# Kernel optimization log

Measured on AMD Instinct MI355X. Metric: run time of the kernel, lower is better.

Reference implementation:

```python
import jax, jax.numpy as jnp
from jax import lax
import numpy as np

DIM = 8          # per-head dim
BN_EPS = 1e-5
ATT_EPS = 1e-15


def setup_inputs() -> dict:
    key = jax.random.key(0)
    ks = jax.random.split(key, 6)
    B, C, H, W = 2, 512, 128, 128
    total_dim = 512                      # heads(64) * dim(8)
    c3 = 3 * total_dim                   # 1536
    x = jax.random.normal(ks[0], (B, C, H, W), dtype=jnp.float32)
    w_qkv = jax.random.normal(ks[1], (c3, C), dtype=jnp.float32) * 0.02
    w_dw = jax.random.normal(ks[2], (c3, 1, 5, 5), dtype=jnp.float32) * 0.05
    w_pw = jax.random.normal(ks[3], (c3, 8, 1, 1), dtype=jnp.float32) * 0.1
    w_proj = jax.random.normal(ks[4], (512, 2 * total_dim), dtype=jnp.float32) * 0.02
    bn_gamma = jnp.ones((512,), jnp.float32)
    bn_beta = jnp.zeros((512,), jnp.float32)
    bn_mean = jnp.zeros((512,), jnp.float32)
    bn_var = jnp.ones((512,), jnp.float32)
    return {"x": x, "w_qkv": w_qkv, "w_dw": w_dw, "w_pw": w_pw, "w_proj": w_proj,
            "bn_gamma": bn_gamma, "bn_beta": bn_beta, "bn_mean": bn_mean, "bn_var": bn_var}


def reference(x, w_qkv, w_dw, w_pw, w_proj, bn_gamma, bn_beta, bn_mean, bn_var):
    B, C, H, W = x.shape
    dn = ('NCHW', 'OIHW', 'NCHW')
    # qkv: 1x1 conv, no bias/norm/act
    qkv = jnp.einsum('bchw,oc->bohw', x, w_qkv)  # (B, 1536, H, W)
    # multi-scale aggregation: 5x5 depthwise + 1x1 grouped (groups = 3*heads = 192)
    y = lax.conv_general_dilated(qkv, w_dw, (1, 1), [(2, 2), (2, 2)],
                                 feature_group_count=w_dw.shape[0], dimension_numbers=dn)
    y = lax.conv_general_dilated(y, w_pw, (1, 1), [(0, 0), (0, 0)],
                                 feature_group_count=w_pw.shape[0] // w_pw.shape[1],
                                 dimension_numbers=dn)
    mqkv = jnp.concatenate([qkv, y], axis=1)  # (B, 3072, H, W)
    N = H * W
    mqkv = mqkv.reshape(B, -1, 3 * DIM, N)    # (B, 128 heads, 24, N)
    q = jax.nn.relu(mqkv[:, :, :DIM])          # (B, h, d, N)
    k = jax.nn.relu(mqkv[:, :, DIM:2 * DIM])   # (B, h, d, N)
    v = mqkv[:, :, 2 * DIM:]                   # (B, h, d, N)
    v = jnp.pad(v, ((0, 0), (0, 0), (0, 1), (0, 0)), constant_values=1.0)  # (B,h,d+1,N)
    vk = jnp.einsum('bhdn,bhen->bhde', v, k)   # v @ k^T : (B,h,d+1,d)
    out = jnp.einsum('bhde,bhen->bhdn', vk, q)  # (B,h,d+1,N)
    out = out[:, :, :-1] / (out[:, :, -1:] + ATT_EPS)  # (B,h,d,N)
    out = out.reshape(B, -1, H, W)             # (B, 1024, H, W)
    # proj: 1x1 conv + bn2d (inference-mode affine), no act
    out = jnp.einsum('bchw,oc->bohw', out, w_proj)
    inv = bn_gamma / jnp.sqrt(bn_var + BN_EPS)
    out = out * inv[None, :, None, None] + (bn_beta - bn_mean * inv)[None, :, None, None]
    return out
```

## Files before the change

### kernel.cpp

```cpp
#include <hip/hip_runtime.h>

typedef __bf16 bf16_t;
typedef __bf16 bf16x8 __attribute__((ext_vector_type(8)));
typedef float  f32x4  __attribute__((ext_vector_type(4)));
typedef _Float16 h16;
typedef _Float16 h16x2 __attribute__((ext_vector_type(2)));
typedef _Float16 h16x4 __attribute__((ext_vector_type(4)));
typedef _Float16 h16x8 __attribute__((ext_vector_type(8)));

#define DEVINL __device__ __forceinline__

static constexpr size_t N_PIX = 16384;
static constexpr float  FIX_TAU = 2.5e-3f;

static constexpr size_t OFF_QB  = 0;
static constexpr size_t SZ_QB   = (size_t)512 * N_PIX * 2;
static constexpr size_t OFF_KV  = OFF_QB + SZ_QB;
static constexpr size_t SZ_KV   = (size_t)1024 * N_PIX * 2;
static constexpr size_t OFF_Y   = OFF_KV + SZ_KV;
static constexpr size_t SZ_Y    = (size_t)1536 * N_PIX * 2;
static constexpr size_t OFF_ATT = OFF_Y + SZ_Y;
static constexpr size_t SZ_ATT  = (size_t)N_PIX * 1024 * 2;
static constexpr size_t OFF_XT  = OFF_ATT;
static constexpr size_t OFF_XTL = OFF_ATT + (size_t)N_PIX * 512 * 2;
static constexpr size_t OFF_WALL= OFF_ATT + SZ_ATT;
static constexpr size_t SZ_WALL = (size_t)1536 * 512 * 2;
static constexpr size_t OFF_WP  = OFF_WALL + SZ_WALL;
static constexpr size_t SZ_WP   = (size_t)512 * 1024 * 2;
static constexpr size_t OFF_VK  = OFF_WP + SZ_WP;
static constexpr size_t SZ_VK   = (size_t)128 * 72 * 4;
static constexpr size_t OFF_VKP = OFF_VK + SZ_VK;
static constexpr size_t SZ_VKP  = (size_t)128 * 8 * 72 * 4;
static constexpr size_t OFF_BNA = OFF_VKP + SZ_VKP;
static constexpr size_t OFF_ZP  = OFF_BNA + 2048;
static constexpr size_t OFF_W2  = OFF_ZP + 64;
static constexpr size_t SZ_W2   = (size_t)512 * 1024 * 2;
static constexpr size_t WS_NEEDED = OFF_W2 + SZ_W2;

DEVINL void gload16(const void* g, void* l) {
  __builtin_amdgcn_global_load_lds((const __attribute__((address_space(1))) void*)g,
                                   (__attribute__((address_space(3))) void*)l, 16, 0, 0);
}

__global__ __launch_bounds__(256)
void xpose_kernel(const float* __restrict__ x, h16* __restrict__ xT, h16* __restrict__ xTl) {
  __shared__ float t[32][33];
  const int n0 = blockIdx.x * 32, c0 = blockIdx.y * 32;
  const int tx = threadIdx.x & 31, ty = threadIdx.x >> 5;
#pragma unroll
  for (int r = 0; r < 4; ++r)
    t[ty + r * 8][tx] = x[(size_t)(c0 + ty + r * 8) * N_PIX + n0 + tx];
  __syncthreads();
  const int nl = threadIdx.x >> 3, sub = threadIdx.x & 7;
  const int c8 = (sub & 3) * 8, plane = sub >> 2;
  h16x8 o;
#pragma unroll
  for (int k = 0; k < 8; ++k) {
    const float v = t[c8 + k][nl];
    if (plane == 0) {
      o[k] = (h16)v;
    } else {
      const h16 hi = (h16)v;
      o[k] = (h16)(v - (float)hi);
    }
  }
  h16* dst = plane ? xTl : xT;
  *(h16x8*)&dst[(size_t)(n0 + nl) * 512 + c0 + c8] = o;
}

static constexpr int PREP_P1 = 1536 * 512;
static constexpr int PREP_P2 = 512 * 1024;
static constexpr int PREP_TOT = PREP_P1 + PREP_P2 + 512 + 16;
__global__ __launch_bounds__(256)
void prep_kernel(const float* __restrict__ wq, const float* __restrict__ wp,
                 const float* __restrict__ gam, const float* __restrict__ bet,
                 const float* __restrict__ mu, const float* __restrict__ va,
                 h16* __restrict__ wall, bf16_t* __restrict__ wpb,
                 float* __restrict__ bna, float* __restrict__ zp) {
  const int i = blockIdx.x * 256 + threadIdx.x;
  if (i < PREP_P1) {
    const int r = i >> 9, c = i & 511;
    int o;
    if (r < 512)       o = (r >> 3) * 24 + (r & 7);
    else if (r < 1024) o = ((r - 512) >> 3) * 24 + 8 + (r & 7);
    else               o = ((r - 1024) >> 3) * 24 + 16 + (r & 7);
    wall[i] = (h16)wq[(size_t)o * 512 + c];
  } else if (i < PREP_P1 + PREP_P2) {
    const int j = i - PREP_P1;
    const int m = j >> 10;
    const float inv = gam[m] / sqrtf(va[m] + 1e-5f);
    wpb[j] = (bf16_t)(wp[j] * inv);
  } else if (i < PREP_P1 + PREP_P2 + 512) {
    const int k = i - PREP_P1 - PREP_P2;
    const float inv = gam[k] / sqrtf(va[k] + 1e-5f);
    bna[k] = bet[k] - mu[k] * inv;
  } else if (i < PREP_TOT) {
    zp[i - (PREP_P1 + PREP_P2 + 512)] = 0.f;
  }
}

__global__ __launch_bounds__(256, 2)
void gemm_qkv_kernel(const h16* __restrict__ wall, const h16* __restrict__ xT,
                     h16* __restrict__ Qb, h16* __restrict__ KV) {
  __shared__ __align__(16) h16 As[128 * 64];
  __shared__ __align__(16) h16 Bs[256 * 64];
  const int tid = threadIdx.x, wid = tid >> 6, lane = tid & 63;
  const int fr = lane & 15, fg = lane >> 4;
  const int wm = (wid >> 1) * 64, wn = (wid & 1) * 128;
  const int by = blockIdx.y;
  const bool isQ = by < 4;
  const int m0 = (isQ ? by : by - 4) * 128;
  const int n0 = blockIdx.x * 256;
  const h16* Aptr = wall + (size_t)by * 128 * 512;

  f32x4 acc[4][8] = {};

  for (int kk = 0; kk < 512; kk += 64) {
    __syncthreads();
#pragma unroll
    for (int r = 0; r < 4; ++r) {
      const int c = wid * 64 + lane + 256 * r;
      const int row = c >> 3, cc = c & 7;
      gload16(Aptr + (size_t)row * 512 + kk + ((cc ^ (row & 7)) * 8),
              As + (size_t)(wid * 64 + 256 * r) * 8);
    }
#pragma unroll
    for (int r = 0; r < 8; ++r) {
      const int c = wid * 64 + lane + 256 * r;
      const int row = c >> 3, cc = c & 7;
      gload16(xT + (size_t)(n0 + row) * 512 + kk + ((cc ^ (row & 7)) * 8),
              Bs + (size_t)(wid * 64 + 256 * r) * 8);
    }
    __syncthreads();
#pragma unroll
    for (int ks = 0; ks < 2; ++ks) {
      h16x8 af[4], bfr[8];
#pragma unroll
      for (int i = 0; i < 4; ++i)
        af[i]  = *(const h16x8*)&As[(wm + i * 16 + fr) * 64 + (((ks * 4 + fg) ^ (fr & 7)) * 8)];
#pragma unroll
      for (int j = 0; j < 8; ++j)
        bfr[j] = *(const h16x8*)&Bs[(wn + j * 16 + fr) * 64 + (((ks * 4 + fg) ^ (fr & 7)) * 8)];
#pragma unroll
      for (int i = 0; i < 4; ++i)
#pragma unroll
        for (int j = 0; j < 8; ++j)
          acc[i][j] = __builtin_amdgcn_mfma_f32_16x16x32_f16(af[i], bfr[j], acc[i][j], 0, 0, 0);
    }
  }

#pragma unroll
  for (int i = 0; i < 4; ++i)
#pragma unroll
    for (int r = 0; r < 4; ++r) {
      const int m = m0 + wm + i * 16 + fg * 4 + r;
      h16* dst = isQ ? Qb : KV;
#pragma unroll
      for (int j = 0; j < 8; ++j) {
        const int n = n0 + wn + j * 16 + fr;
        dst[(size_t)m * N_PIX + n] = (h16)acc[i][j][r];
      }
    }
}

__global__ __launch_bounds__(256)
void fix_kernel(const float* __restrict__ wq, const h16* __restrict__ xT,
                const h16* __restrict__ xTl, h16* __restrict__ Qb) {
  const int h = blockIdx.y;
  const int n = blockIdx.x * 256 + threadIdx.x;
  const int lane = threadIdx.x & 63;
  float mx = 0.f;
#pragma unroll
  for (int e = 0; e < 8; ++e)
    mx = fmaxf(mx, (float)Qb[(size_t)(h * 8 + e) * N_PIX + n]);
  unsigned long long mask = __ballot(mx < FIX_TAU);
  const int cb = blockIdx.x * 256 + ((int)threadIdx.x & ~63);
  while (mask) {
    const int bit = __builtin_ctzll(mask);
    mask &= mask - 1;
    const int np = cb + bit;
    const int c0 = lane * 8;
    const h16x8 xh = *(const h16x8*)&xT[(size_t)np * 512 + c0];
    const h16x8 xl = *(const h16x8*)&xTl[(size_t)np * 512 + c0];
    float xs[8];
#pragma unroll
    for (int u = 0; u < 8; ++u) xs[u] = (float)xh[u] + (float)xl[u];
    float acc[8];
#pragma unroll
    for (int e = 0; e < 8; ++e) {
      const float4 w0 = *(const float4*)&wq[(size_t)(h * 24 + e) * 512 + c0];
      const float4 w1 = *(const float4*)&wq[(size_t)(h * 24 + e) * 512 + c0 + 4];
      acc[e] = w0.x * xs[0] + w0.y * xs[1] + w0.z * xs[2] + w0.w * xs[3]
             + w1.x * xs[4] + w1.y * xs[5] + w1.z * xs[6] + w1.w * xs[7];
    }
#pragma unroll
    for (int e = 0; e < 8; ++e) {
      acc[e] += __shfl_xor(acc[e], 32); acc[e] += __shfl_xor(acc[e], 16);
      acc[e] += __shfl_xor(acc[e], 8);  acc[e] += __shfl_xor(acc[e], 4);
      acc[e] += __shfl_xor(acc[e], 2);  acc[e] += __shfl_xor(acc[e], 1);
    }
    if (lane < 8) {
      float v = acc[0];
#pragma unroll
      for (int e = 1; e < 8; ++e) if (lane == e) v = acc[e];
      Qb[(size_t)(h * 8 + lane) * N_PIX + np] = (h16)v;
    }
  }
}

__global__ __launch_bounds__(256, 4)
void gemm_proj_kernel(const bf16_t* __restrict__ A, const bf16_t* __restrict__ B,
                      float* __restrict__ Cout, const float* __restrict__ bna) {
  __shared__ __align__(16) bf16_t As[128 * 64];
  __shared__ __align__(16) bf16_t Bs[128 * 64];
  const int tid = threadIdx.x, wid = tid >> 6, lane = tid & 63;
  const int fr = lane & 15, fg = lane >> 4;
  const int wm = (wid >> 1) * 64, wn = (wid & 1) * 64;
  const int m0 = blockIdx.y * 128, n0 = blockIdx.x * 128;
  const int srow = tid >> 3;
  const int soff = (((tid & 7) ^ (srow & 7)) * 8);
  const bf16_t* Ab = A + (size_t)m0 * 1024;
  const bf16_t* Bb = B + (size_t)n0 * 1024;

  f32x4 acc[4][4] = {};

  for (int kk = 0; kk < 1024; kk += 64) {
    __syncthreads();
#pragma unroll
    for (int r = 0; r < 4; ++r) {
      gload16(Ab + (size_t)(srow + 32 * r) * 1024 + kk + soff, As + (wid * 8 + 32 * r) * 64);
      gload16(Bb + (size_t)(srow + 32 * r) * 1024 + kk + soff, Bs + (wid * 8 + 32 * r) * 64);
    }
    __syncthreads();
#pragma unroll
    for (int ks = 0; ks < 2; ++ks) {
      bf16x8 af[4], bfr[4];
#pragma unroll
      for (int i = 0; i < 4; ++i)
        af[i]  = *(const bf16x8*)&As[(wm + i * 16 + fr) * 64 + (((ks * 4 + fg) ^ (fr & 7)) * 8)];
#pragma unroll
      for (int j = 0; j < 4; ++j)
        bfr[j] = *(const bf16x8*)&Bs[(wn + j * 16 + fr) * 64 + (((ks * 4 + fg) ^ (fr & 7)) * 8)];
#pragma unroll
      for (int i = 0; i < 4; ++i)
#pragma unroll
        for (int j = 0; j < 4; ++j)
          acc[i][j] = __builtin_amdgcn_mfma_f32_16x16x32_bf16(af[i], bfr[j], acc[i][j], 0, 0, 0);
    }
  }

#pragma unroll
  for (int i = 0; i < 4; ++i)
#pragma unroll
    for (int r = 0; r < 4; ++r) {
      const int m = m0 + wm + i * 16 + fg * 4 + r;
      const float sh = bna[m];
#pragma unroll
      for (int j = 0; j < 4; ++j)
        Cout[(size_t)m * N_PIX + n0 + wn + j * 16 + fr] = acc[i][j][r] + sh;
    }
}

__global__ __launch_bounds__(256)
void dwpw_kernel(const h16* __restrict__ Qb, const h16* __restrict__ KV,
                 const float* __restrict__ wdw, const float* __restrict__ wpw,
                 const h16* __restrict__ zp, h16* __restrict__ y) {
  const int bidHW = blockIdx.x + (blockIdx.y << 4);
  const int work  = (bidHW & 7) * 384 + (bidHW >> 3);
  const int g = work >> 4, t = work & 15;
  const int typ = g % 3, head = g / 3;
  const int ty0 = (t >> 1) * 16, tx0 = (t & 1) * 64;
  const int tid = threadIdx.x, wid = tid >> 6, lane = tid & 63;
  __shared__ __align__(16) h16 sin_[8][20][80];
  __shared__ h16x2 swd2[8][25];
  __shared__ h16x2 swp2[8][8];
  if (tid < 200) {
    const h16 w = (h16)wdw[(g * 8 + tid / 25) * 25 + tid % 25];
    h16x2 w2; w2[0] = w; w2[1] = w;
    swd2[tid / 25][tid % 25] = w2;
  }
  if (tid < 64) {
    const h16 w = (h16)wpw[(g * 8 + (tid >> 3)) * 8 + (tid & 7)];
    h16x2 w2; w2[0] = w; w2[1] = w;
    swp2[tid >> 3][tid & 7] = w2;
  }
  const h16* plane = (typ == 0) ? (Qb + (size_t)head * 8 * N_PIX)
                                : (KV + (size_t)((typ == 2 ? 512 : 0) + head * 8) * N_PIX);
  h16* sflat = &sin_[0][0][0];

  auto stageChunk = [&](int id) {
    const int ch  = id / 200;
    const int rem = id - ch * 200;
    const int row = rem / 10;
    const int c6  = rem - row * 10;
    const int gy  = ty0 + row - 2;
    const int gx  = tx0 + c6 * 8 - 8;
    const bool ok = ((unsigned)gy < 128u) && ((unsigned)gx < 128u);
    const h16* src = ok ? (plane + (size_t)ch * N_PIX + gy * 128 + gx) : zp;
    gload16(src, sflat + (size_t)id * 8);
  };

  for (int base = wid * 64; base < 832; base += 256) stageChunk(base + lane);
  __syncthreads();
  for (int base = 832 + wid * 64; base < 1600; base += 256) stageChunk(base + lane);

  const int px4 = (tid & 15) * 4, py = tid >> 4;
  h16x2 dwa[8][2];

  auto dwCh = [&](int ch) {
    h16x2 A0 = 0, A1 = 0;
#pragma unroll
    for (int di = 0; di < 5; ++di) {
      const uint2 w0 = *(const uint2*)&sin_[ch][py + di][px4 + 4];
      const uint2 w1 = *(const uint2*)&sin_[ch][py + di][px4 + 8];
      const uint2 w2v = *(const uint2*)&sin_[ch][py + di][px4 + 12];
      const unsigned u1 = w0.y, u2 = w1.x, u3 = w1.y, u4 = w2v.x;
      const h16x2 P2 = __builtin_bit_cast(h16x2, u1);
      const h16x2 P3 = __builtin_bit_cast(h16x2, (u2 << 16) | (u1 >> 16));
      const h16x2 P4 = __builtin_bit_cast(h16x2, u2);
      const h16x2 P5 = __builtin_bit_cast(h16x2, (u3 << 16) | (u2 >> 16));
      const h16x2 P6 = __builtin_bit_cast(h16x2, u3);
      const h16x2 P7 = __builtin_bit_cast(h16x2, (u4 << 16) | (u3 >> 16));
      const h16x2 P8 = __builtin_bit_cast(h16x2, u4);
      h16x2 wd;
      wd = swd2[ch][di * 5 + 0]; A0 += wd * P2; A1 += wd * P4;
      wd = swd2[ch][di * 5 + 1]; A0 += wd * P3; A1 += wd * P5;
      wd = swd2[ch][di * 5 + 2]; A0 += wd * P4; A1 += wd * P6;
      wd = swd2[ch][di * 5 + 3]; A0 += wd * P5; A1 += wd * P7;
      wd = swd2[ch][di * 5 + 4]; A0 += wd * P6; A1 += wd * P8;
    }
    dwa[ch][0] = A0; dwa[ch][1] = A1;
  };

#pragma unroll
  for (int ch = 0; ch < 4; ++ch) dwCh(ch);
  __syncthreads();
#pragma unroll
  for (int ch = 4; ch < 8; ++ch) dwCh(ch);

#pragma unroll
  for (int oc = 0; oc < 8; ++oc) {
    h16x2 o0 = 0, o1 = 0;
#pragma unroll
    for (int ic = 0; ic < 8; ++ic) {
      const h16x2 w = swp2[oc][ic];
      o0 += w * dwa[ic][0];
      o1 += w * dwa[ic][1];
    }
    h16x4 ov; ov[0] = o0[0]; ov[1] = o0[1]; ov[2] = o1[0]; ov[3] = o1[1];
    *(h16x4*)&y[(size_t)(8 * g + oc) * N_PIX + (ty0 + py) * 128 + tx0 + px4] = ov;
  }
}

__global__ __launch_bounds__(256)
void vk_partial_kernel(const h16* __restrict__ KV, const h16* __restrict__ yb,
                       float* __restrict__ part) {
  const int h = blockIdx.y, s = blockIdx.x;
  const h16 *kb, *vb;
  if (h < 64) {
    kb = KV + (size_t)(h * 8) * N_PIX;
    vb = KV + (size_t)(512 + h * 8) * N_PIX;
  } else {
    kb = yb + (size_t)(24 * (h - 64) + 8) * N_PIX;
    vb = yb + (size_t)(24 * (h - 64) + 16) * N_PIX;
  }
  float a[8][8] = {};
  float ak[8] = {};
  const int p0 = s * 2048 + (int)threadIdx.x * 8;
  float kq[8][8], vq[8][8];
#pragma unroll
  for (int e = 0; e < 8; ++e) {
    h16x8 kk = *(const h16x8*)&kb[(size_t)e * N_PIX + p0];
#pragma unroll
    for (int u = 0; u < 8; ++u) kq[e][u] = fmaxf(0.f, (float)kk[u]);
  }
#pragma unroll
  for (int d = 0; d < 8; ++d) {
    h16x8 vv = *(const h16x8*)&vb[(size_t)d * N_PIX + p0];
#pragma unroll
    for (int u = 0; u < 8; ++u) vq[d][u] = (float)vv[u];
  }
#pragma unroll
  for (int d = 0; d < 8; ++d)
#pragma unroll
    for (int e = 0; e < 8; ++e)
#pragma unroll
      for (int u = 0; u < 8; ++u) a[d][e] += vq[d][u] * kq[e][u];
#pragma unroll
  for (int e = 0; e < 8; ++e)
#pragma unroll
    for (int u = 0; u < 8; ++u) ak[e] += kq[e][u];

  __shared__ float red[4][72];
  const int lane = threadIdx.x & 63, wid = threadIdx.x >> 6;
#pragma unroll
  for (int i = 0; i < 72; ++i) {
    float v = (i < 64) ? a[i >> 3][i & 7] : ak[i - 64];
    v += __shfl_xor(v, 32); v += __shfl_xor(v, 16); v += __shfl_xor(v, 8);
    v += __shfl_xor(v, 4);  v += __shfl_xor(v, 2);  v += __shfl_xor(v, 1);
    if (lane == 0) red[wid][i] = v;
  }
  __syncthreads();
  if (threadIdx.x < 72) {
    const float sum_ = red[0][threadIdx.x] + red[1][threadIdx.x] + red[2][threadIdx.x] + red[3][threadIdx.x];
    part[((size_t)h * 8 + s) * 72 + threadIdx.x] = sum_;
  }
}

__global__ __launch_bounds__(128)
void vk_reduce_kernel(const float* __restrict__ part, float* __restrict__ vk) {
  const int h = blockIdx.x;
  const int i = threadIdx.x;
  if (i < 72) {
    float s = 0.f;
#pragma unroll
    for (int t = 0; t < 8; ++t) s += part[((size_t)h * 8 + t) * 72 + i];
    vk[(size_t)h * 72 + i] = s;
  }
}

__global__ __launch_bounds__(256)
void w2_kernel(const bf16_t* __restrict__ wpb, const float* __restrict__ vkm,
               bf16_t* __restrict__ W2) {
  const int idx = blockIdx.x * 256 + threadIdx.x;
  const int m = idx >> 10, c = idx & 1023;
  const int h = c >> 3, e = c & 7;
  float s = 0.f;
#pragma unroll
  for (int d = 0; d < 8; ++d)
    s += (float)wpb[(size_t)m * 1024 + h * 8 + d] * vkm[h * 72 + d * 8 + e];
  W2[idx] = (bf16_t)s;
}

__global__ __launch_bounds__(256)
void qn_kernel(const h16* __restrict__ Qb, const h16* __restrict__ yb,
               const float* __restrict__ vk, bf16_t* __restrict__ qnT) {
  const int n0 = blockIdx.x * 32;
  const int tid = threadIdx.x;
  const int px = tid & 31, hl = tid >> 5;
  __shared__ __align__(16) bf16_t att_s[32 * 512];
  __shared__ float ak_all[128][8];
#pragma unroll
  for (int r = 0; r < 4; ++r) {
    const int i = tid + r * 256;
    ak_all[i >> 3][i & 7] = vk[(size_t)(i >> 3) * 72 + 64 + (i & 7)];
  }
  __syncthreads();
  for (int grp = 0; grp < 2; ++grp) {
    for (int hg = 0; hg < 8; ++hg) {
      const int hh = hg * 8 + hl;
      const int habs = grp * 64 + hh;
      float q[8];
      if (grp == 0) {
        const h16* plane = Qb + (size_t)(hh * 8) * N_PIX + n0 + px;
#pragma unroll
        for (int e = 0; e < 8; ++e) q[e] = fmaxf(0.f, (float)plane[(size_t)e * N_PIX]);
      } else {
        const h16* plane = yb + (size_t)(24 * hh) * N_PIX + n0 + px;
#pragma unroll
        for (int e = 0; e < 8; ++e) q[e] = fmaxf(0.f, (float)plane[(size_t)e * N_PIX]);
      }
      float den = 1e-15f;
#pragma unroll
      for (int e = 0; e < 8; ++e) den += ak_all[habs][e] * q[e];
      const float rden = 1.0f / den;
      bf16x8 r8;
#pragma unroll
      for (int e = 0; e < 8; ++e) r8[e] = (bf16_t)(q[e] * rden);
      const int chunk = hg * 8 + hl;
      *(bf16x8*)&att_s[px * 512 + ((chunk ^ (px & 7)) << 3)] = r8;
    }
    __syncthreads();
    bf16_t* dst = qnT + (size_t)n0 * 1024 + grp * 512;
    for (int i = tid; i < 2048; i += 256) {
      const int r = i >> 6, cc = i & 63;
      bf16x8 v = *(const bf16x8*)&att_s[r * 512 + (((cc ^ (r & 7))) << 3)];
      *(bf16x8*)&dst[(size_t)r * 1024 + cc * 8] = v;
    }
    __syncthreads();
  }
}

extern "C" void kernel_launch(void* const* d_in, const int* in_sizes, int n_in,
                              void* d_out, int out_size, void* d_ws, size_t ws_size,
                              hipStream_t stream) {
  if (ws_size < WS_NEEDED) return;
  const float* x      = (const float*)d_in[0];
  const float* w_qkv  = (const float*)d_in[1];
  const float* w_dw   = (const float*)d_in[2];
  const float* w_pw   = (const float*)d_in[3];
  const float* w_proj = (const float*)d_in[4];
  const float* gam    = (const float*)d_in[5];
  const float* bet    = (const float*)d_in[6];
  const float* mu     = (const float*)d_in[7];
  const float* va     = (const float*)d_in[8];

  char* w = (char*)d_ws;
  h16*    Qb   = (h16*)(w + OFF_QB);
  h16*    KV   = (h16*)(w + OFF_KV);
  h16*    yb   = (h16*)(w + OFF_Y);
  h16*    xT   = (h16*)(w + OFF_XT);
  h16*    xTl  = (h16*)(w + OFF_XTL);
  bf16_t* qnT  = (bf16_t*)(w + OFF_ATT);
  h16*    wall = (h16*)(w + OFF_WALL);
  bf16_t* wpb  = (bf16_t*)(w + OFF_WP);
  bf16_t* W2   = (bf16_t*)(w + OFF_W2);
  float*  vk   = (float*)(w + OFF_VK);
  float*  part = (float*)(w + OFF_VKP);
  float*  bna  = (float*)(w + OFF_BNA);
  float*  zp   = (float*)(w + OFF_ZP);

  dim3 blk(256);
  prep_kernel<<<dim3((PREP_TOT + 255) / 256), blk, 0, stream>>>(
      w_qkv, w_proj, gam, bet, mu, va, wall, wpb, bna, zp);

  for (int b = 0; b < 2; ++b) {
    const float* xb = x + (size_t)b * 512 * N_PIX;
    float* outb = (float*)d_out + (size_t)b * 512 * N_PIX;
    xpose_kernel<<<dim3(512, 16), blk, 0, stream>>>(xb, xT, xTl);
    gemm_qkv_kernel<<<dim3(64, 12), blk, 0, stream>>>(wall, xT, Qb, KV);
    fix_kernel<<<dim3(64, 64), blk, 0, stream>>>(w_qkv, xT, xTl, Qb);
    dwpw_kernel<<<dim3(16, 192), blk, 0, stream>>>(Qb, KV, w_dw, w_pw, (const h16*)zp, yb);
    vk_partial_kernel<<<dim3(8, 128), blk, 0, stream>>>(KV, yb, part);
    vk_reduce_kernel<<<dim3(128), dim3(128), 0, stream>>>(part, vk);
    w2_kernel<<<dim3(512 * 1024 / 256), blk, 0, stream>>>(wpb, vk, W2);
    qn_kernel<<<dim3(512), blk, 0, stream>>>(Qb, yb, vk, qnT);
    gemm_proj_kernel<<<dim3(128, 4), blk, 0, stream>>>(W2, qnT, outb, bna);
  }
}
```

Baseline: 324.2 us.

## Double-buffer QKV GEMM shared tiles and shrink N tile to 128

```diff
diff --git a/kernel.cpp b/kernel.cpp
--- a/kernel.cpp
+++ b/kernel.cpp
@@ -102,51 +102,52 @@
 __global__ __launch_bounds__(256, 2)
 void gemm_qkv_kernel(const h16* __restrict__ wall, const h16* __restrict__ xT,
                      h16* __restrict__ Qb, h16* __restrict__ KV) {
-  __shared__ __align__(16) h16 As[128 * 64];
-  __shared__ __align__(16) h16 Bs[256 * 64];
+  __shared__ __align__(16) h16 As[2][128 * 64];
+  __shared__ __align__(16) h16 Bs[2][128 * 64];
   const int tid = threadIdx.x, wid = tid >> 6, lane = tid & 63;
   const int fr = lane & 15, fg = lane >> 4;
-  const int wm = (wid >> 1) * 64, wn = (wid & 1) * 128;
+  const int wm = (wid >> 1) * 64, wn = (wid & 1) * 64;
   const int by = blockIdx.y;
   const bool isQ = by < 4;
   const int m0 = (isQ ? by : by - 4) * 128;
-  const int n0 = blockIdx.x * 256;
+  const int n0 = blockIdx.x * 128;
   const h16* Aptr = wall + (size_t)by * 128 * 512;
-
-  f32x4 acc[4][8] = {};
-
+  const h16* Bptr = xT + (size_t)n0 * 512;
+  const int srow = tid >> 3;
+  const int soff = (((tid & 7) ^ (srow & 7)) * 8);
+
+  auto stage = [&](int kk, int buf) {
+#pragma unroll
+    for (int r = 0; r < 4; ++r) {
+      gload16(Aptr + (size_t)(srow + 32 * r) * 512 + kk + soff, &As[buf][(wid * 8 + 32 * r) * 64]);
+      gload16(Bptr + (size_t)(srow + 32 * r) * 512 + kk + soff, &Bs[buf][(wid * 8 + 32 * r) * 64]);
+    }
+  };
+
+  f32x4 acc[4][4] = {};
+
+  stage(0, 0);
+  __syncthreads();
+  int cur = 0;
   for (int kk = 0; kk < 512; kk += 64) {
+    if (kk + 64 < 512) stage(kk + 64, cur ^ 1);
+#pragma unroll
+    for (int ks = 0; ks < 2; ++ks) {
+      h16x8 af[4], bfr[4];
+#pragma unroll
+      for (int i = 0; i < 4; ++i)
+        af[i]  = *(const h16x8*)&As[cur][(wm + i * 16 + fr) * 64 + (((ks * 4 + fg) ^ (fr & 7)) * 8)];
+#pragma unroll
+      for (int j = 0; j < 4; ++j)
+        bfr[j] = *(const h16x8*)&Bs[cur][(wn + j * 16 + fr) * 64 + (((ks * 4 + fg) ^ (fr & 7)) * 8)];
+#pragma unroll
+      for (int i = 0; i < 4; ++i)
+#pragma unroll
+        for (int j = 0; j < 4; ++j)
+          acc[i][j] = __builtin_amdgcn_mfma_f32_16x16x32_f16(af[i], bfr[j], acc[i][j], 0, 0, 0);
+    }
     __syncthreads();
-#pragma unroll
-    for (int r = 0; r < 4; ++r) {
-      const int c = wid * 64 + lane + 256 * r;
-      const int row = c >> 3, cc = c & 7;
-      gload16(Aptr + (size_t)row * 512 + kk + ((cc ^ (row & 7)) * 8),
-              As + (size_t)(wid * 64 + 256 * r) * 8);
-    }
-#pragma unroll
-    for (int r = 0; r < 8; ++r) {
-      const int c = wid * 64 + lane + 256 * r;
-      const int row = c >> 3, cc = c & 7;
-      gload16(xT + (size_t)(n0 + row) * 512 + kk + ((cc ^ (row & 7)) * 8),
-              Bs + (size_t)(wid * 64 + 256 * r) * 8);
-    }
-    __syncthreads();
-#pragma unroll
-    for (int ks = 0; ks < 2; ++ks) {
-      h16x8 af[4], bfr[8];
-#pragma unroll
-      for (int i = 0; i < 4; ++i)
-        af[i]  = *(const h16x8*)&As[(wm + i * 16 + fr) * 64 + (((ks * 4 + fg) ^ (fr & 7)) * 8)];
-#pragma unroll
-      for (int j = 0; j < 8; ++j)
-        bfr[j] = *(const h16x8*)&Bs[(wn + j * 16 + fr) * 64 + (((ks * 4 + fg) ^ (fr & 7)) * 8)];
-#pragma unroll
-      for (int i = 0; i < 4; ++i)
-#pragma unroll
-        for (int j = 0; j < 8; ++j)
-          acc[i][j] = __builtin_amdgcn_mfma_f32_16x16x32_f16(af[i], bfr[j], acc[i][j], 0, 0, 0);
-    }
+    cur ^= 1;
   }
 
 #pragma unroll
@@ -156,7 +157,7 @@
       const int m = m0 + wm + i * 16 + fg * 4 + r;
       h16* dst = isQ ? Qb : KV;
 #pragma unroll
-      for (int j = 0; j < 8; ++j) {
+      for (int j = 0; j < 4; ++j) {
         const int n = n0 + wn + j * 16 + fr;
         dst[(size_t)m * N_PIX + n] = (h16)acc[i][j][r];
       }
@@ -518,7 +519,7 @@
     const float* xb = x + (size_t)b * 512 * N_PIX;
     float* outb = (float*)d_out + (size_t)b * 512 * N_PIX;
     xpose_kernel<<<dim3(512, 16), blk, 0, stream>>>(xb, xT, xTl);
-    gemm_qkv_kernel<<<dim3(64, 12), blk, 0, stream>>>(wall, xT, Qb, KV);
+    gemm_qkv_kernel<<<dim3(128, 12), blk, 0, stream>>>(wall, xT, Qb, KV);
     fix_kernel<<<dim3(64, 64), blk, 0, stream>>>(w_qkv, xT, xTl, Qb);
     dwpw_kernel<<<dim3(16, 192), blk, 0, stream>>>(Qb, KV, w_dw, w_pw, (const h16*)zp, yb);
     vk_partial_kernel<<<dim3(8, 128), blk, 0, stream>>>(KV, yb, part);
```

After: 322.1 us, median of 2. About the same (-0.7%).
